# Kernel optimization log

Measured on AMD Instinct MI355X. Metric: run time of the kernel, lower is better.

The kernel has to match this reference:

```python
import jax, jax.numpy as jnp
import numpy as np

_LAP = jnp.array([[0., 1., 0.], [1., -4., 1.], [0., 1., 0.]], dtype=jnp.float32).reshape(1, 1, 3, 3)  # OIHW

def _laplacian(x):
    # x: [B,1,H,W]; SAME padding (pad=1), stride 1
    return jax.lax.conv_general_dilated(
        x, _LAP, window_strides=(1, 1), padding=((1, 1), (1, 1)),
        dimension_numbers=('NCHW', 'OIHW', 'NCHW'))

def setup_inputs() -> dict:
    key = jax.random.key(0)
    k1, k2 = jax.random.split(key)
    B, C, H, W = 16, 1, 1024, 1024
    pred = jax.random.normal(k1, (B, C, H, W), dtype=jnp.float32)
    target = jax.random.normal(k2, (B, C, H, W), dtype=jnp.float32)
    mask = jnp.ones((B, C, H, W), dtype=jnp.float32)
    return {"pred": pred, "target": target, "mask": mask}

def reference(pred, target, mask):
    # Laplacian curvature of pred and target; note conv is linear so this
    # equals laplacian(pred - target), but we keep the original two-conv math.
    pred_curv = _laplacian(pred)
    target_curv = _laplacian(target)
    loss = jnp.abs(pred_curv - target_curv) * mask
    return loss.sum() / (mask.sum() + 1e-8)
```

## Files before the change

kernel.cpp:

```cpp
#include <hip/hip_runtime.h>


static constexpr int IMG_W = 1024;
static constexpr int IMG_H = 1024;
static constexpr int TH_ROWS = 16;
static constexpr int NT = 256;

__global__ __launch_bounds__(NT) void curv_partial_kernel(
    const float* __restrict__ pred,
    const float* __restrict__ target,
    const float* __restrict__ mask,
    float* __restrict__ partial,
    int H)
{
    __shared__ float sd[3][IMG_W];
    __shared__ float wls[NT / 64], wms[NT / 64];

    const int tid = threadIdx.x;
    const int blocksPerImage = H / TH_ROWS;
    const int b  = blockIdx.x / blocksPerImage;
    const int y0 = (blockIdx.x % blocksPerImage) * TH_ROWS;
    const size_t imgOff = (size_t)b * H * IMG_W;
    const int x4 = tid * 4;

    float lsum = 0.f, msum = 0.f;

    auto loadRow = [&](int y, int slot) {
        float4 d;
        if (y >= 0 && y < H) {
            const size_t o = imgOff + (size_t)y * IMG_W + x4;
            const float4 p = *reinterpret_cast<const float4*>(pred + o);
            const float4 t = *reinterpret_cast<const float4*>(target + o);
            d = make_float4(p.x - t.x, p.y - t.y, p.z - t.z, p.w - t.w);
        } else {
            d = make_float4(0.f, 0.f, 0.f, 0.f);
        }
        *reinterpret_cast<float4*>(&sd[slot][x4]) = d;
    };

    loadRow(y0 - 1, 0);
    loadRow(y0,     1);

    for (int r = 0; r < TH_ROWS; ++r) {
        const int y = y0 + r;
        loadRow(y + 1, (r + 2) % 3);
        __syncthreads();

        const float* up = sd[r % 3];
        const float* ce = sd[(r + 1) % 3];
        const float* dn = sd[(r + 2) % 3];

        const float4 m = *reinterpret_cast<const float4*>(mask + imgOff + (size_t)y * IMG_W + x4);

        const float c0 = ce[x4], c1 = ce[x4 + 1], c2 = ce[x4 + 2], c3 = ce[x4 + 3];
        const float left  = (x4 == 0)         ? 0.f : ce[x4 - 1];
        const float right = (x4 + 4 == IMG_W) ? 0.f : ce[x4 + 4];

        const float l0 = up[x4]     + dn[x4]     + left + c1    - 4.f * c0;
        const float l1 = up[x4 + 1] + dn[x4 + 1] + c0   + c2    - 4.f * c1;
        const float l2 = up[x4 + 2] + dn[x4 + 2] + c1   + c3    - 4.f * c2;
        const float l3 = up[x4 + 3] + dn[x4 + 3] + c2   + right - 4.f * c3;

        lsum += fabsf(l0) * m.x + fabsf(l1) * m.y + fabsf(l2) * m.z + fabsf(l3) * m.w;
        msum += m.x + m.y + m.z + m.w;

        __syncthreads();
    }

    for (int off = 32; off > 0; off >>= 1) {
        lsum += __shfl_down(lsum, off, 64);
        msum += __shfl_down(msum, off, 64);
    }
    const int wave = tid >> 6;
    if ((tid & 63) == 0) { wls[wave] = lsum; wms[wave] = msum; }
    __syncthreads();
    if (tid == 0) {
        float L = 0.f, M = 0.f;
        #pragma unroll
        for (int w = 0; w < NT / 64; ++w) { L += wls[w]; M += wms[w]; }
        partial[2 * (size_t)blockIdx.x]     = L;
        partial[2 * (size_t)blockIdx.x + 1] = M;
    }
}

__global__ __launch_bounds__(256) void curv_final_kernel(
    const float* __restrict__ partial, float* __restrict__ out, int nblocks)
{
    __shared__ float sL[256], sM[256];
    float L = 0.f, M = 0.f;
    for (int i = threadIdx.x; i < nblocks; i += 256) {
        L += partial[2 * (size_t)i];
        M += partial[2 * (size_t)i + 1];
    }
    sL[threadIdx.x] = L; sM[threadIdx.x] = M;
    __syncthreads();
    for (int s = 128; s > 0; s >>= 1) {
        if (threadIdx.x < s) {
            sL[threadIdx.x] += sL[threadIdx.x + s];
            sM[threadIdx.x] += sM[threadIdx.x + s];
        }
        __syncthreads();
    }
    if (threadIdx.x == 0) out[0] = sL[0] / (sM[0] + 1e-8f);
}

extern "C" void kernel_launch(void* const* d_in, const int* in_sizes, int n_in,
                              void* d_out, int out_size, void* d_ws, size_t ws_size,
                              hipStream_t stream) {
    const float* pred   = (const float*)d_in[0];
    const float* target = (const float*)d_in[1];
    const float* mask   = (const float*)d_in[2];
    float* out = (float*)d_out;
    float* partial = (float*)d_ws;

    const int H = IMG_H;
    const int B = in_sizes[0] / (IMG_H * IMG_W);
    const int nblocks = B * (H / TH_ROWS);

    curv_partial_kernel<<<nblocks, NT, 0, stream>>>(pred, target, mask, partial, H);
    curv_final_kernel<<<1, 256, 0, stream>>>(partial, out, nblocks);
}
```

Baseline: 38.54 us.

## Replace shared-memory row ring with register rolling and wave shuffles

Drops the shared-memory three-row ring buffer and its two barriers per row. Vertical neighbours now roll through registers, horizontal neighbours come from cross-lane shuffles, and the lanes at each wave edge load their halo element directly from global memory. Rows per block drop from 16 to 8 and the row loop is fully unrolled, which doubles the block count and adds more halo-row reloads. This targets barrier stalls and LDS traffic, at the cost of extra global reads at block and wave boundaries.

```diff
diff --git a/kernel.cpp b/kernel.cpp
--- a/kernel.cpp
+++ b/kernel.cpp
@@ -3,8 +3,8 @@
 
 static constexpr int IMG_W = 1024;
 static constexpr int IMG_H = 1024;
-static constexpr int TH_ROWS = 16;
-static constexpr int NT = 256;
+static constexpr int ROWS  = 8;
+static constexpr int NT    = 256;
 
 __global__ __launch_bounds__(NT) void curv_partial_kernel(
     const float* __restrict__ pred,
@@ -13,66 +13,68 @@
     float* __restrict__ partial,
     int H)
 {
-    __shared__ float sd[3][IMG_W];
-    __shared__ float wls[NT / 64], wms[NT / 64];
-
-    const int tid = threadIdx.x;
-    const int blocksPerImage = H / TH_ROWS;
+    const int tid  = threadIdx.x;
+    const int lane = tid & 63;
+    const int blocksPerImage = H / ROWS;
     const int b  = blockIdx.x / blocksPerImage;
-    const int y0 = (blockIdx.x % blocksPerImage) * TH_ROWS;
+    const int y0 = (blockIdx.x % blocksPerImage) * ROWS;
     const size_t imgOff = (size_t)b * H * IMG_W;
     const int x4 = tid * 4;
 
+    auto loadD = [&](int y) -> float4 {
+        if (y < 0 || y >= H) return make_float4(0.f, 0.f, 0.f, 0.f);
+        const size_t o = imgOff + (size_t)y * IMG_W + x4;
+        const float4 p = *reinterpret_cast<const float4*>(pred + o);
+        const float4 t = *reinterpret_cast<const float4*>(target + o);
+        return make_float4(p.x - t.x, p.y - t.y, p.z - t.z, p.w - t.w);
+    };
+
+    float4 d_prev = loadD(y0 - 1);
+    float4 d_cur  = loadD(y0);
+
     float lsum = 0.f, msum = 0.f;
 
-    auto loadRow = [&](int y, int slot) {
-        float4 d;
-        if (y >= 0 && y < H) {
-            const size_t o = imgOff + (size_t)y * IMG_W + x4;
-            const float4 p = *reinterpret_cast<const float4*>(pred + o);
-            const float4 t = *reinterpret_cast<const float4*>(target + o);
-            d = make_float4(p.x - t.x, p.y - t.y, p.z - t.z, p.w - t.w);
-        } else {
-            d = make_float4(0.f, 0.f, 0.f, 0.f);
+    #pragma unroll
+    for (int r = 0; r < ROWS; ++r) {
+        const int y = y0 + r;
+        const float4 d_next = loadD(y + 1);
+
+        float eL = 0.f, eR = 0.f;
+        if (lane == 0 && x4 != 0) {
+            const size_t o = imgOff + (size_t)y * IMG_W + (x4 - 1);
+            eL = pred[o] - target[o];
         }
-        *reinterpret_cast<float4*>(&sd[slot][x4]) = d;
-    };
+        if (lane == 63 && x4 + 4 != IMG_W) {
+            const size_t o = imgOff + (size_t)y * IMG_W + (x4 + 4);
+            eR = pred[o] - target[o];
+        }
 
-    loadRow(y0 - 1, 0);
-    loadRow(y0,     1);
-
-    for (int r = 0; r < TH_ROWS; ++r) {
-        const int y = y0 + r;
-        loadRow(y + 1, (r + 2) % 3);
-        __syncthreads();
-
-        const float* up = sd[r % 3];
-        const float* ce = sd[(r + 1) % 3];
-        const float* dn = sd[(r + 2) % 3];
+        float left  = __shfl_up(d_cur.w, 1, 64);
+        float right = __shfl_down(d_cur.x, 1, 64);
+        if (lane == 0)  left  = eL;
+        if (lane == 63) right = eR;
 
         const float4 m = *reinterpret_cast<const float4*>(mask + imgOff + (size_t)y * IMG_W + x4);
 
-        const float c0 = ce[x4], c1 = ce[x4 + 1], c2 = ce[x4 + 2], c3 = ce[x4 + 3];
-        const float left  = (x4 == 0)         ? 0.f : ce[x4 - 1];
-        const float right = (x4 + 4 == IMG_W) ? 0.f : ce[x4 + 4];
-
-        const float l0 = up[x4]     + dn[x4]     + left + c1    - 4.f * c0;
-        const float l1 = up[x4 + 1] + dn[x4 + 1] + c0   + c2    - 4.f * c1;
-        const float l2 = up[x4 + 2] + dn[x4 + 2] + c1   + c3    - 4.f * c2;
-        const float l3 = up[x4 + 3] + dn[x4 + 3] + c2   + right - 4.f * c3;
+        const float l0 = d_prev.x + d_next.x + left    + d_cur.y - 4.f * d_cur.x;
+        const float l1 = d_prev.y + d_next.y + d_cur.x + d_cur.z - 4.f * d_cur.y;
+        const float l2 = d_prev.z + d_next.z + d_cur.y + d_cur.w - 4.f * d_cur.z;
+        const float l3 = d_prev.w + d_next.w + d_cur.z + right   - 4.f * d_cur.w;
 
         lsum += fabsf(l0) * m.x + fabsf(l1) * m.y + fabsf(l2) * m.z + fabsf(l3) * m.w;
         msum += m.x + m.y + m.z + m.w;
 
-        __syncthreads();
+        d_prev = d_cur;
+        d_cur  = d_next;
     }
 
     for (int off = 32; off > 0; off >>= 1) {
         lsum += __shfl_down(lsum, off, 64);
         msum += __shfl_down(msum, off, 64);
     }
+    __shared__ float wls[NT / 64], wms[NT / 64];
     const int wave = tid >> 6;
-    if ((tid & 63) == 0) { wls[wave] = lsum; wms[wave] = msum; }
+    if (lane == 0) { wls[wave] = lsum; wms[wave] = msum; }
     __syncthreads();
     if (tid == 0) {
         float L = 0.f, M = 0.f;
@@ -115,7 +117,7 @@
 
     const int H = IMG_H;
     const int B = in_sizes[0] / (IMG_H * IMG_W);
-    const int nblocks = B * (H / TH_ROWS);
+    const int nblocks = B * (H / ROWS);
 
     curv_partial_kernel<<<nblocks, NT, 0, stream>>>(pred, target, mask, partial, H);
     curv_final_kernel<<<1, 256, 0, stream>>>(partial, out, nblocks);
```

Result: slower. 43.56 us (+13.0%).
